# Optimization experiments

Measured on AMD Instinct MI355X. Metric: run time of the kernel, lower is better.

Reference implementation:

```python
import jax, jax.numpy as jnp
import numpy as np

REG_MAX = 16
NUM_CLASSES = 1
NUM_KPTS = 17
TOPK = 13
EPS = 1e-9

OKS_SIGMAS = np.array([0.026,0.025,0.025,0.035,0.035,0.079,0.079,0.072,0.072,0.062,0.062,0.107,0.107,0.087,0.087,0.089,0.089], np.float32)


def _bce(logits, target):
    # stable binary_cross_entropy_with_logits, reduction='none'
    return jnp.maximum(logits, 0.0) - logits * target + jnp.log1p(jnp.exp(-jnp.abs(logits)))


def _pairwise_iou(gt, pred):
    # gt [B,n,4], pred [B,L,4] -> iou [B,n,L]
    g = gt[:, :, None, :]
    p = pred[:, None, :, :]
    inter_w = jnp.clip(jnp.minimum(g[..., 2], p[..., 2]) - jnp.maximum(g[..., 0], p[..., 0]), 0.0)
    inter_h = jnp.clip(jnp.minimum(g[..., 3], p[..., 3]) - jnp.maximum(g[..., 1], p[..., 1]), 0.0)
    inter = inter_w * inter_h
    ag = (g[..., 2] - g[..., 0]) * (g[..., 3] - g[..., 1])
    ap = (p[..., 2] - p[..., 0]) * (p[..., 3] - p[..., 1])
    return inter / (ag + ap - inter + EPS)


def _assign(pred_scores_sig, pred_bboxes, anchor_points, gt_class, gt_bboxes, pad_gt_mask):
    # TaskAlignedAssigner(topk=13, alpha=1.0, beta=6.0)
    B, n, _ = gt_bboxes.shape
    L = pred_bboxes.shape[1]
    ious = _pairwise_iou(gt_bboxes, pred_bboxes)                                  # [B,n,L]
    idx = jnp.broadcast_to(gt_class, (B, n, L))
    cls = jnp.take_along_axis(jnp.swapaxes(pred_scores_sig, 1, 2), idx, axis=1)   # [B,n,L]
    metrics = cls * ious ** 6.0                                                   # alpha=1, beta=6
    ap = anchor_points[None, None, :, :]
    in_gt = ((ap[..., 0] - gt_bboxes[:, :, None, 0] > EPS)
             & (ap[..., 1] - gt_bboxes[:, :, None, 1] > EPS)
             & (gt_bboxes[:, :, None, 2] - ap[..., 0] > EPS)
             & (gt_bboxes[:, :, None, 3] - ap[..., 1] > EPS)).astype(metrics.dtype)
    _, topk_idx = jax.lax.top_k(metrics * in_gt, TOPK)                            # [B,n,K]
    topk_idx = jnp.where(pad_gt_mask > 0, topk_idx, 0)
    is_in_topk = jax.nn.one_hot(topk_idx, L, dtype=metrics.dtype).sum(-2)
    is_in_topk = jnp.where(is_in_topk > 1, 0.0, is_in_topk)
    mask_pos = is_in_topk * in_gt * pad_gt_mask                                   # [B,n,L]
    # resolve anchors assigned to multiple gts: keep gt with max iou
    is_max_iou = jnp.swapaxes(jax.nn.one_hot(ious.argmax(axis=1), n, dtype=metrics.dtype), 1, 2)
    mask_pos = jnp.where(mask_pos.sum(1, keepdims=True) > 1, is_max_iou, mask_pos)
    pos = mask_pos.sum(1) > 0                                                     # [B,L]
    assigned_gt_index = mask_pos.argmax(1)                                        # [B,L]
    bix = jnp.arange(B)[:, None]
    assigned_labels = jnp.where(pos, gt_class[bix, assigned_gt_index, 0], NUM_CLASSES)
    assigned_bboxes = gt_bboxes[bix, assigned_gt_index]                           # [B,L,4]
    one_hot_lbl = jax.nn.one_hot(assigned_labels, NUM_CLASSES + 1, dtype=metrics.dtype)[..., :NUM_CLASSES]
    # rescale alignment metrics by per-gt max iou / max metric
    m = metrics * mask_pos
    m = m / (m.max(-1, keepdims=True) + EPS) * (ious * mask_pos).max(-1, keepdims=True)
    assigned_scores = one_hot_lbl * m.max(1)[..., None]                           # [B,L,1]
    return assigned_labels, assigned_bboxes, assigned_scores, assigned_gt_index, pos


def _bbox_decode(anchor_points_s, pred_distri):
    B, L, _ = pred_distri.shape
    prob = jax.nn.softmax(pred_distri.reshape(B, L, 4, REG_MAX + 1), axis=-1)
    dist = prob @ jnp.arange(REG_MAX + 1, dtype=prob.dtype)                       # DFL projection
    return jnp.concatenate([anchor_points_s - dist[..., :2], anchor_points_s + dist[..., 2:]], -1)


def _giou(pb, gb):
    inter_w = jnp.clip(jnp.minimum(pb[..., 2], gb[..., 2]) - jnp.maximum(pb[..., 0], gb[..., 0]), 0.0)
    inter_h = jnp.clip(jnp.minimum(pb[..., 3], gb[..., 3]) - jnp.maximum(pb[..., 1], gb[..., 1]), 0.0)
    inter = inter_w * inter_h
    a1 = (pb[..., 2] - pb[..., 0]) * (pb[..., 3] - pb[..., 1])
    a2 = (gb[..., 2] - gb[..., 0]) * (gb[..., 3] - gb[..., 1])
    union = a1 + a2 - inter + EPS
    iou = inter / union
    cw = jnp.maximum(pb[..., 2], gb[..., 2]) - jnp.minimum(pb[..., 0], gb[..., 0])
    ch = jnp.maximum(pb[..., 3], gb[..., 3]) - jnp.minimum(pb[..., 1], gb[..., 1])
    area_c = cw * ch + EPS
    return 1.0 - (iou - (area_c - union) / area_c)


def _df_loss(pred_dist, target):
    # pred_dist [B,L,4,reg_max+1], target [B,L,4] in [0, reg_max-0.01]
    tl = jnp.floor(target).astype(jnp.int32)
    wl = (tl.astype(target.dtype) + 1.0) - target
    logp = jax.nn.log_softmax(pred_dist, -1)
    ll = -jnp.take_along_axis(logp, tl[..., None], -1)[..., 0]
    lr = -jnp.take_along_axis(logp, (tl + 1)[..., None], -1)[..., 0]
    return (ll * wl + lr * (1.0 - wl)).mean(-1)                                   # [B,L]


def _forward(pred_scores, pred_distri, pred_pose_logits, anchor_points, stride_tensor,
             gt_bboxes, pad_gt_mask, gt_poses, oks_sigmas, gt_class):
    B, L, _ = pred_scores.shape
    anchor_points_s = anchor_points / stride_tensor
    pred_bboxes = _bbox_decode(anchor_points_s, pred_distri)
    sgd = jax.lax.stop_gradient
    assigned_labels, assigned_bboxes, assigned_scores, assigned_gt_index, pos = _assign(
        sgd(jax.nn.sigmoid(pred_scores)), sgd(pred_bboxes * stride_tensor), anchor_points,
        gt_class, gt_bboxes, pad_gt_mask)
    assigned_bboxes = assigned_bboxes / stride_tensor
    # focal classification loss (alpha=-1 -> no alpha weighting, gamma=2)
    w = jnp.abs(jax.nn.sigmoid(pred_scores) - assigned_scores) ** 2
    ass_sum = jnp.maximum(assigned_scores.sum(), 1.0)
    loss_cls = (w * _bce(pred_scores, assigned_scores)).sum() / ass_sum
    posf = pos.astype(pred_scores.dtype)
    bbox_w = assigned_scores.sum(-1) * posf                                        # [B,L]
    loss_iou = (_giou(pred_bboxes, assigned_bboxes) * bbox_w).sum() / ass_sum
    ltrb = jnp.clip(jnp.concatenate([anchor_points_s - assigned_bboxes[..., :2],
                                     assigned_bboxes[..., 2:] - anchor_points_s], -1),
                    0.0, REG_MAX - 0.01)
    loss_dfl = (_df_loss(pred_distri.reshape(B, L, 4, REG_MAX + 1), ltrb) * bbox_w).sum() / ass_sum
    bix = jnp.arange(B)[:, None]
    kpts = gt_poses[bix, assigned_gt_index]                                        # [B,L,J,3]
    gt_xy = kpts[..., :2] / stride_tensor[None, :, None, :]
    pred_xy = pred_pose_logits[..., :2] + anchor_points_s[None, :, None, :]
    d = ((pred_xy - gt_xy) ** 2).sum(-1)                                           # [B,L,J]
    kmf = ((kpts[..., 2] != 0) & pos[..., None]).astype(d.dtype)
    area = ((assigned_bboxes[..., 2] - assigned_bboxes[..., 0])
            * (assigned_bboxes[..., 3] - assigned_bboxes[..., 1]))[..., None]
    e = d / (2.0 * oks_sigmas[None, None, :]) ** 2 / (area + EPS) / 2.0
    n_pos_kpts = jnp.maximum(posf.sum() * NUM_KPTS, 1.0)
    factor = n_pos_kpts / (kmf.sum() + EPS)
    loss_pose_reg = factor * ((1.0 - jnp.exp(-e)) * kmf).sum() / n_pos_kpts
    loss_pose_cls = (_bce(pred_pose_logits[..., 2], kmf) * posf[..., None]).sum() / n_pos_kpts
    loss = 1.0 * loss_cls + 2.5 * loss_iou + 0.5 * loss_dfl + 1.0 * loss_pose_cls + 1.0 * loss_pose_reg
    log_losses = jnp.stack([loss_cls, loss_iou, loss_dfl, loss_pose_cls, loss_pose_reg, loss])
    return loss, log_losses


def _make_anchors():
    pts, strides = [], []
    for s in (8, 16, 32):
        g = 640 // s
        xs = (np.arange(g, dtype=np.float32) + 0.5) * s
        yv, xv = np.meshgrid(xs, xs, indexing='ij')
        pts.append(np.stack([xv.ravel(), yv.ravel()], -1))
        strides.append(np.full((g * g, 1), s, np.float32))
    return jnp.asarray(np.concatenate(pts)), jnp.asarray(np.concatenate(strides))


def setup_inputs() -> dict:
    B, N, J, L = 16, 32, 17, 8400
    key = jax.random.key(0)
    ks = jax.random.split(key, 8)
    anchor_points, stride_tensor = _make_anchors()
    x1y1 = jax.random.uniform(ks[0], (B, N, 2), minval=0.0, maxval=480.0)
    wh = jax.random.uniform(ks[1], (B, N, 2), minval=32.0, maxval=160.0)
    gt_bboxes = jnp.concatenate([x1y1, x1y1 + wh], -1)
    pad_gt_mask = jnp.broadcast_to((jnp.arange(N)[None, :, None] < 24), (B, N, 1)).astype(jnp.float32)
    gt_class = jnp.zeros((B, N, 1), jnp.int32)
    ctr = x1y1 + wh / 2.0
    kxy = ctr[:, :, None, :] + jax.random.normal(ks[2], (B, N, J, 2)) * wh[:, :, None, :] * 0.2
    vis = jax.random.randint(ks[3], (B, N, J), 0, 3).astype(jnp.float32)
    gt_poses = jnp.concatenate([kxy, vis[..., None]], -1)
    pred_scores = jax.random.normal(ks[4], (B, L, 1)) * 0.5 - 2.0
    pred_distri = jax.random.normal(ks[5], (B, L, 4 * (REG_MAX + 1)))
    pred_pose_logits = jax.random.normal(ks[6], (B, L, J, 3))
    return {'pred_scores': pred_scores, 'pred_distri': pred_distri,
            'pred_pose_logits': pred_pose_logits, 'anchor_points': anchor_points,
            'stride_tensor': stride_tensor, 'gt_bboxes': gt_bboxes,
            'pad_gt_mask': pad_gt_mask, 'gt_poses': gt_poses,
            'oks_sigmas': jnp.asarray(OKS_SIGMAS), 'gt_class': gt_class}


def reference(pred_scores, pred_distri, pred_pose_logits, anchor_points, stride_tensor,
              gt_bboxes, pad_gt_mask, gt_poses, oks_sigmas, gt_class):
    return _forward(pred_scores, pred_distri, pred_pose_logits, anchor_points, stride_tensor,
                    gt_bboxes, pad_gt_mask, gt_poses, oks_sigmas, gt_class)
```

## Files before the change

### kernel.cpp

```cpp
#include <hip/hip_runtime.h>
#include <cstddef>

#define EPS 1e-9f
#define REG_MAX 16
#define TOPK 13
#define NGT 32
#define CAP 1024
#define LSLOT 16

__device__ __forceinline__ float sigmoidf(float x){ return 1.0f/(1.0f+expf(-x)); }
__device__ __forceinline__ float bcef(float l, float t){
    return fmaxf(l,0.0f) - l*t + log1pf(expf(-fabsf(l)));
}
__device__ __forceinline__ float pow6f(float x){ float x2=x*x; return x2*x2*x2; }
__device__ __forceinline__ float iou_px(float p0,float p1,float p2,float p3,
                                        float4 g, float gag){
    float iw = fmaxf(fminf(g.z,p2)-fmaxf(g.x,p0), 0.f);
    float ih = fmaxf(fminf(g.w,p3)-fmaxf(g.y,p1), 0.f);
    float inter = iw*ih;
    float ap = (p2-p0)*(p3-p1);
    return inter/(gag+ap-inter+EPS);
}

__global__ void k_zero(int* __restrict__ ccnt, unsigned int* __restrict__ rowmax_m,
                       unsigned int* __restrict__ rowmax_i, int* __restrict__ pcnt,
                       int BN)
{
    int t = threadIdx.x;
    for (int i=t; i<BN; i+=256){ ccnt[i]=0; rowmax_m[i]=0u; rowmax_i[i]=0u; }
    if (t==0) *pcnt = 0;
}

__global__ void k_main(const float* __restrict__ pred_scores,
                       const float* __restrict__ pred_distri,
                       const float* __restrict__ anchor_points,
                       const float* __restrict__ stride_t,
                       const float* __restrict__ gt_bboxes,
                       const float* __restrict__ pad_mask,
                       float* __restrict__ pred_bboxes,
                       float* __restrict__ sig_g,
                       unsigned int* __restrict__ words,
                       float2* __restrict__ cand,
                       int* __restrict__ ccnt,
                       int B,int N,int L,int nchunks)
{
    __shared__ float4 sgt[NGT];
    __shared__ float  sag[NGT];
    __shared__ int    sval[NGT];
    int b = blockIdx.x / nchunks, chunk = blockIdx.x % nchunks;
    int tid = threadIdx.x;
    if (tid < N){
        float4 g = ((const float4*)gt_bboxes)[b*N+tid];
        sgt[tid] = g;
        sag[tid] = (g.z-g.x)*(g.w-g.y);
        sval[tid] = pad_mask[b*N+tid] > 0.f ? 1 : 0;
    }
    __syncthreads();
    int l = chunk*256 + tid;
    if (l >= L) return;
    int idx = b*L + l;
    words[idx] = 0u;

    float v[68];
    const float4* pd4 = (const float4*)(pred_distri + (size_t)idx*68);
    #pragma unroll
    for (int i=0;i<17;i++){ float4 q = pd4[i]; v[4*i]=q.x; v[4*i+1]=q.y; v[4*i+2]=q.z; v[4*i+3]=q.w; }
    float dist[4];
    #pragma unroll
    for (int s=0;s<4;s++){
        float m = -1e30f;
        #pragma unroll
        for (int i=0;i<=REG_MAX;i++) m = fmaxf(m, v[s*17+i]);
        float sum=0.f, ws=0.f;
        #pragma unroll
        for (int i=0;i<=REG_MAX;i++){ float e = expf(v[s*17+i]-m); sum+=e; ws += e*(float)i; }
        dist[s] = ws/sum;
    }
    float st = stride_t[l];
    float apx = anchor_points[2*l], apy = anchor_points[2*l+1];
    float ax = apx/st, ay = apy/st;
    float4 box = make_float4(ax-dist[0], ay-dist[1], ax+dist[2], ay+dist[3]);
    ((float4*)pred_bboxes)[idx] = box;
    float sg = sigmoidf(pred_scores[idx]);
    sig_g[idx] = sg;

    float p0 = box.x*st, p1 = box.y*st, p2 = box.z*st, p3 = box.w*st;
    #pragma unroll
    for (int n=0;n<NGT;n++){
        float4 g = sgt[n];
        bool ing = (apx-g.x>EPS)&&(apy-g.y>EPS)&&(g.z-apx>EPS)&&(g.w-apy>EPS);
        if (ing && sval[n]){
            float iou = iou_px(p0,p1,p2,p3,g,sag[n]);
            float mv = sg*pow6f(iou);
            int slot = atomicAdd(&ccnt[b*N+n], 1);
            if (slot < CAP) cand[(size_t)(b*N+n)*CAP+slot] = make_float2(mv, __int_as_float(l));
        }
    }
}

__global__ void k_select(const float2* __restrict__ cand,
                         const int* __restrict__ ccnt,
                         unsigned int* __restrict__ words,
                         int B,int N,int L)
{
    int bn = blockIdx.x; int b = bn/N, n = bn%N;
    int cnt = ccnt[bn]; cnt = cnt < CAP ? cnt : CAP;
    int tid = threadIdx.x;
    unsigned int nbit = 1u<<n;
    const float2* my = cand + (size_t)bn*CAP;
    if (cnt <= TOPK){
        if (tid < cnt) atomicOr(&words[b*L + __float_as_int(my[tid].y)], nbit);
        return;
    }
    if (tid >= 64) return;
    float lv[LSLOT]; int li[LSLOT];
    #pragma unroll
    for (int k=0;k<LSLOT;k++){ lv[k]=-1.f; li[k]=0x7fffffff; }
    for (int i=tid; i<cnt; i+=64){
        float2 e = my[i];
        float cv = e.x; int ci = __float_as_int(e.y);
        #pragma unroll
        for (int k=0;k<LSLOT;k++){
            bool better = (cv>lv[k]) || (cv==lv[k] && ci<li[k]);
            if (better){
                float tv=lv[k]; lv[k]=cv; cv=tv;
                int   ti=li[k]; li[k]=ci; ci=ti;
            }
        }
    }
    for (int r=0;r<TOPK;r++){
        float bv=lv[0]; int bl=li[0];
        #pragma unroll
        for (int off=32; off>0; off>>=1){
            float ov = __shfl_xor(bv, off);
            int   oi = __shfl_xor(bl, off);
            if (ov>bv || (ov==bv && oi<bl)){ bv=ov; bl=oi; }
        }
        if (li[0]==bl){
            atomicOr(&words[b*L + bl], nbit);
            #pragma unroll
            for (int k=0;k<LSLOT-1;k++){ lv[k]=lv[k+1]; li[k]=li[k+1]; }
            lv[LSLOT-1]=-1.f; li[LSLOT-1]=0x7fffffff;
        }
    }
}

__global__ void k_resolve(const float* __restrict__ pred_bboxes,
                          const float* __restrict__ stride_t,
                          const float* __restrict__ gt_bboxes,
                          const float* __restrict__ sig,
                          unsigned int* __restrict__ words,
                          unsigned int* __restrict__ rowmax_m,
                          unsigned int* __restrict__ rowmax_i,
                          int* __restrict__ poslist,
                          int* __restrict__ pcnt,
                          int B,int N,int L)
{
    int idx = blockIdx.x*blockDim.x + threadIdx.x;
    if (idx >= B*L) return;
    int b = idx / L, l = idx % L;
    unsigned int w = words[idx];
    if (!w) return;
    float4 box = ((const float4*)pred_bboxes)[idx];
    float st = stride_t[l];
    float p0 = box.x*st, p1 = box.y*st, p2 = box.z*st, p3 = box.w*st;
    const float4* gt = (const float4*)gt_bboxes + b*N;
    int n;
    if (__popc(w) > 1){
        float bv=-1e30f; int bbest=0;
        #pragma unroll 4
        for (int nn=0;nn<NGT;nn++){
            float4 g = gt[nn];
            float vv = iou_px(p0,p1,p2,p3,g,(g.z-g.x)*(g.w-g.y));
            if (vv > bv){ bv=vv; bbest=nn; }
        }
        n = bbest;
        words[idx] = 1u<<n;
    } else {
        n = __ffs(w)-1;
    }
    float4 g = gt[n];
    float iou = iou_px(p0,p1,p2,p3,g,(g.z-g.x)*(g.w-g.y));
    float met = sig[idx]*pow6f(iou);
    atomicMax(&rowmax_m[b*N+n], __float_as_uint(met));
    atomicMax(&rowmax_i[b*N+n], __float_as_uint(iou));
    int slot = atomicAdd(pcnt, 1);
    poslist[slot] = idx;
}

__global__ void k_loss(const float* __restrict__ pred_scores,
                       const float* __restrict__ pred_distri,
                       const float* __restrict__ pose_logits,
                       const float* __restrict__ anchor_points,
                       const float* __restrict__ stride_t,
                       const float* __restrict__ gt_bboxes,
                       const float* __restrict__ gt_poses,
                       const float* __restrict__ sigmas,
                       const int*   __restrict__ gt_class,
                       const float* __restrict__ pred_bboxes,
                       const float* __restrict__ sig,
                       const unsigned int* __restrict__ words,
                       const unsigned int* __restrict__ rowmax_m,
                       const unsigned int* __restrict__ rowmax_i,
                       const int* __restrict__ poslist,
                       const int* __restrict__ pcnt,
                       float* __restrict__ partials,
                       int B,int N,int L,int J)
{
    int tid = threadIdx.x;
    float a_score=0,a_cls=0,a_giou=0,a_dfl=0,a_pos=0,a_kmf=0,a_preg=0,a_pcls=0;

    int idx = blockIdx.x*blockDim.x + tid;
    if (idx < B*L){
        int b = idx/L, l = idx%L;
        unsigned int w = words[idx];
        float assigned = 0.f;
        if (w){
            int n = __ffs(w)-1;
            float4 box = ((const float4*)pred_bboxes)[idx];
            float st = stride_t[l];
            float4 g = ((const float4*)gt_bboxes)[b*N+n];
            float iou = iou_px(box.x*st,box.y*st,box.z*st,box.w*st,
                               g,(g.z-g.x)*(g.w-g.y));
            float met = sig[idx]*pow6f(iou);
            float score = met/(__uint_as_float(rowmax_m[b*N+n])+EPS)
                          *__uint_as_float(rowmax_i[b*N+n]);
            if (gt_class[b*N+n]==0) assigned = score;
        }
        float logit = pred_scores[idx];
        float sg = sig[idx];
        float wg = sg - assigned; wg *= wg;
        a_cls = wg * bcef(logit, assigned);
        a_score = assigned;
    }

    int cnt = *pcnt;
    int e = blockIdx.x + tid*gridDim.x;
    if (e < cnt){
        int pidx = poslist[e];
        int b = pidx/L, l = pidx%L;
        int n = __ffs(words[pidx])-1;
        float st = stride_t[l];
        float4 pb = ((const float4*)pred_bboxes)[pidx];
        float4 g  = ((const float4*)gt_bboxes)[b*N+n];
        float iou0 = iou_px(pb.x*st,pb.y*st,pb.z*st,pb.w*st,
                            g,(g.z-g.x)*(g.w-g.y));
        float met = sig[pidx]*pow6f(iou0);
        float score = met/(__uint_as_float(rowmax_m[b*N+n])+EPS)
                      *__uint_as_float(rowmax_i[b*N+n]);
        float assigned = (gt_class[b*N+n]==0) ? score : 0.f;
        a_pos = 1.f;
        float ab0=g.x/st, ab1=g.y/st, ab2=g.z/st, ab3=g.w/st;
        float area = (ab2-ab0)*(ab3-ab1);
        float apx = anchor_points[2*l]/st, apy = anchor_points[2*l+1]/st;
        float bw = assigned;
        if (bw > 0.f){
            float iw = fmaxf(fminf(pb.z,ab2)-fmaxf(pb.x,ab0),0.f);
            float ih = fmaxf(fminf(pb.w,ab3)-fmaxf(pb.y,ab1),0.f);
            float inter=iw*ih;
            float a1=(pb.z-pb.x)*(pb.w-pb.y);
            float a2=(ab2-ab0)*(ab3-ab1);
            float uni=a1+a2-inter+EPS;
            float iou=inter/uni;
            float cw=fmaxf(pb.z,ab2)-fminf(pb.x,ab0);
            float ch=fmaxf(pb.w,ab3)-fminf(pb.y,ab1);
            float ac=cw*ch+EPS;
            float gg = 1.f-(iou-(ac-uni)/ac);
            a_giou = gg*bw;
            float t4[4] = { apx-ab0, apy-ab1, ab2-apx, ab3-apy };
            const float* pdist = pred_distri + (size_t)pidx*68;
            const float4* pd4 = (const float4*)pdist;
            float v[68];
            #pragma unroll
            for (int q=0;q<17;q++){ float4 qq=pd4[q]; v[4*q]=qq.x; v[4*q+1]=qq.y; v[4*q+2]=qq.z; v[4*q+3]=qq.w; }
            float dfl=0.f;
            #pragma unroll
            for (int s2=0;s2<4;s2++){
                float tt = fminf(fmaxf(t4[s2],0.f),(float)REG_MAX-0.01f);
                int tl = (int)floorf(tt);
                float wl = (float)tl + 1.f - tt;
                float m=-1e30f;
                #pragma unroll
                for (int q=0;q<=REG_MAX;q++) m=fmaxf(m,v[s2*17+q]);
                float se=0.f;
                #pragma unroll
                for (int q=0;q<=REG_MAX;q++) se+=expf(v[s2*17+q]-m);
                float lse = m + logf(se);
                float ll = -(pdist[s2*17+tl]-lse);
                float lr = -(pdist[s2*17+tl+1]-lse);
                dfl += ll*wl + lr*(1.f-wl);
            }
            a_dfl = dfl*0.25f*bw;
        }
        const float* gp = gt_poses + ((size_t)(b*N+n))*J*3;
        const float* pl = pose_logits + (size_t)pidx*J*3;
        for (int j=0;j<J;j++){
            float gx=gp[3*j]/st, gy=gp[3*j+1]/st, vis=gp[3*j+2];
            float px=pl[3*j]+apx, py=pl[3*j+1]+apy, pz=pl[3*j+2];
            float kmf = (vis!=0.f)?1.f:0.f;
            float dx=px-gx, dy=py-gy;
            float d = dx*dx+dy*dy;
            float s2g = 2.f*sigmas[j]; s2g*=s2g;
            float ee = d/s2g/(area+EPS)/2.f;
            a_preg += (1.f-expf(-ee))*kmf;
            a_kmf  += kmf;
            a_pcls += bcef(pz, kmf);
        }
    }

    float acc[8] = {a_score,a_cls,a_giou,a_dfl,a_pos,a_kmf,a_preg,a_pcls};
    #pragma unroll
    for (int k=0;k<8;k++){
        #pragma unroll
        for (int off=32; off>0; off>>=1) acc[k] += __shfl_xor(acc[k], off);
    }
    __shared__ float wsum[8][8];
    int wid = tid>>6;
    if ((tid&63)==0){
        #pragma unroll
        for (int k=0;k<8;k++) wsum[wid][k]=acc[k];
    }
    __syncthreads();
    if (tid<8){
        float s=0.f;
        #pragma unroll
        for (int i=0;i<8;i++) s += wsum[i][tid];
        partials[(size_t)blockIdx.x*8+tid]=s;
    }
}

__global__ void k_final(const float* __restrict__ partials, int nblk, int J,
                        float* __restrict__ out)
{
    __shared__ float red[256][9];
    int tid = threadIdx.x;
    float acc[8] = {0,0,0,0,0,0,0,0};
    for (int i=tid; i<nblk; i+=256){
        const float4* p = (const float4*)(partials + (size_t)i*8);
        float4 a = p[0], b = p[1];
        acc[0]+=a.x; acc[1]+=a.y; acc[2]+=a.z; acc[3]+=a.w;
        acc[4]+=b.x; acc[5]+=b.y; acc[6]+=b.z; acc[7]+=b.w;
    }
    #pragma unroll
    for (int k=0;k<8;k++) red[tid][k]=acc[k];
    __syncthreads();
    for (int s=128;s>0;s>>=1){
        if (tid<s){
            #pragma unroll
            for (int k=0;k<8;k++) red[tid][k]+=red[tid+s][k];
        }
        __syncthreads();
    }
    if (tid==0){
        float ass  = fmaxf(red[0][0],1.f);
        float lcls = red[0][1]/ass;
        float liou = red[0][2]/ass;
        float ldfl = red[0][3]/ass;
        float npk  = fmaxf(red[0][4]*(float)J,1.f);
        float factor = npk/(red[0][5]+EPS);
        float preg = factor*red[0][6]/npk;
        float pcls = red[0][7]/npk;
        float loss = lcls + 2.5f*liou + 0.5f*ldfl + pcls + preg;
        out[0]=loss; out[1]=lcls; out[2]=liou; out[3]=ldfl;
        out[4]=pcls; out[5]=preg; out[6]=loss;
    }
}

extern "C" void kernel_launch(void* const* d_in, const int* in_sizes, int n_in,
                              void* d_out, int out_size, void* d_ws, size_t ws_size,
                              hipStream_t stream)
{
    const float* pred_scores   = (const float*)d_in[0];
    const float* pred_distri   = (const float*)d_in[1];
    const float* pose_logits   = (const float*)d_in[2];
    const float* anchor_points = (const float*)d_in[3];
    const float* stride_t      = (const float*)d_in[4];
    const float* gt_bboxes     = (const float*)d_in[5];
    const float* pad_mask      = (const float*)d_in[6];
    const float* gt_poses      = (const float*)d_in[7];
    const float* sigmas        = (const float*)d_in[8];
    const int*   gt_class      = (const int*)d_in[9];

    int L = in_sizes[3]/2;
    int B = in_sizes[0]/L;
    int N = in_sizes[5]/(B*4);
    int J = in_sizes[8];

    char* ws = (char*)d_ws;
    size_t off=0;
    auto alloc=[&](size_t bytes)->void*{
        size_t cur=off; off += (bytes+255)/256*256; return (void*)(ws+cur);
    };
    float* pred_bboxes    = (float*)alloc((size_t)B*L*4*4);
    float* sig            = (float*)alloc((size_t)B*L*4);
    unsigned int* words   = (unsigned int*)alloc((size_t)B*L*4);
    unsigned int* rowmax_m= (unsigned int*)alloc((size_t)B*N*4);
    unsigned int* rowmax_i= (unsigned int*)alloc((size_t)B*N*4);
    float2* cand          = (float2*)alloc((size_t)B*N*CAP*8);
    int* ccnt             = (int*)alloc((size_t)B*N*4);
    int maxpos = B*N*TOPK;
    int* poslist          = (int*)alloc((size_t)maxpos*4);
    int* pcnt             = (int*)alloc(256);
    int nchunks  = (L+255)/256;
    int nblkR    = (B*L+255)/256;
    int nblkL    = (B*L+511)/512;
    float* partials       = (float*)alloc((size_t)nblkL*8*4);
    (void)ws_size; (void)n_in; (void)out_size;

    k_zero<<<1,256,0,stream>>>(ccnt,rowmax_m,rowmax_i,pcnt,B*N);
    k_main<<<B*nchunks,256,0,stream>>>(pred_scores,pred_distri,anchor_points,
                                       stride_t,gt_bboxes,pad_mask,
                                       pred_bboxes,sig,words,cand,ccnt,
                                       B,N,L,nchunks);
    k_select<<<B*N,256,0,stream>>>(cand,ccnt,words,B,N,L);
    k_resolve<<<nblkR,256,0,stream>>>(pred_bboxes,stride_t,gt_bboxes,sig,
                                      words,rowmax_m,rowmax_i,
                                      poslist,pcnt,B,N,L);
    k_loss<<<nblkL,512,0,stream>>>(pred_scores,pred_distri,pose_logits,
                                   anchor_points,stride_t,gt_bboxes,gt_poses,
                                   sigmas,gt_class,pred_bboxes,sig,
                                   words,rowmax_m,rowmax_i,poslist,pcnt,
                                   partials,B,N,L,J);
    k_final<<<1,256,0,stream>>>(partials,nblkL,J,(float*)d_out);
}
```

Baseline: 97.77 us.

## Replace global candidate atomics with per-block segmented lists and fuse final reduction

Candidate collection in the main kernel now uses wave ballots and per-block shared counters, writing into per-chunk segments instead of global atomics on one list per gt. The select kernel prefix-sums the chunk counts and also does the zeroing that a separate kernel used to do. The final reduction is folded into the loss kernel with a last-block ticket, and the loss block size changes to 256. These remove two launches and global atomic contention, at the cost of a serial prefix scan per gt and a linear segment search per element. The segment capacity of 256 is tied to the 256-thread chunk size.

```diff
diff --git a/kernel.cpp b/kernel.cpp
--- a/kernel.cpp
+++ b/kernel.cpp
@@ -5,7 +5,7 @@
 #define REG_MAX 16
 #define TOPK 13
 #define NGT 32
-#define CAP 1024
+#define SEGCAP 256
 #define LSLOT 16
 
 __device__ __forceinline__ float sigmoidf(float x){ return 1.0f/(1.0f+expf(-x)); }
@@ -20,15 +20,6 @@
     float inter = iw*ih;
     float ap = (p2-p0)*(p3-p1);
     return inter/(gag+ap-inter+EPS);
-}
-
-__global__ void k_zero(int* __restrict__ ccnt, unsigned int* __restrict__ rowmax_m,
-                       unsigned int* __restrict__ rowmax_i, int* __restrict__ pcnt,
-                       int BN)
-{
-    int t = threadIdx.x;
-    for (int i=t; i<BN; i+=256){ ccnt[i]=0; rowmax_m[i]=0u; rowmax_i[i]=0u; }
-    if (t==0) *pcnt = 0;
 }
 
 __global__ void k_main(const float* __restrict__ pred_scores,
@@ -40,84 +31,119 @@
                        float* __restrict__ pred_bboxes,
                        float* __restrict__ sig_g,
                        unsigned int* __restrict__ words,
-                       float2* __restrict__ cand,
-                       int* __restrict__ ccnt,
+                       float2* __restrict__ cand2,
+                       int* __restrict__ cnts2,
                        int B,int N,int L,int nchunks)
 {
     __shared__ float4 sgt[NGT];
     __shared__ float  sag[NGT];
     __shared__ int    sval[NGT];
-    int b = blockIdx.x / nchunks, chunk = blockIdx.x % nchunks;
+    __shared__ int    lcnt[NGT];
+    int bc = blockIdx.x;
+    int b = bc / nchunks, chunk = bc % nchunks;
     int tid = threadIdx.x;
     if (tid < N){
         float4 g = ((const float4*)gt_bboxes)[b*N+tid];
         sgt[tid] = g;
         sag[tid] = (g.z-g.x)*(g.w-g.y);
         sval[tid] = pad_mask[b*N+tid] > 0.f ? 1 : 0;
+        lcnt[tid] = 0;
     }
     __syncthreads();
     int l = chunk*256 + tid;
-    if (l >= L) return;
-    int idx = b*L + l;
-    words[idx] = 0u;
-
-    float v[68];
-    const float4* pd4 = (const float4*)(pred_distri + (size_t)idx*68);
-    #pragma unroll
-    for (int i=0;i<17;i++){ float4 q = pd4[i]; v[4*i]=q.x; v[4*i+1]=q.y; v[4*i+2]=q.z; v[4*i+3]=q.w; }
-    float dist[4];
-    #pragma unroll
-    for (int s=0;s<4;s++){
-        float m = -1e30f;
-        #pragma unroll
-        for (int i=0;i<=REG_MAX;i++) m = fmaxf(m, v[s*17+i]);
-        float sum=0.f, ws=0.f;
-        #pragma unroll
-        for (int i=0;i<=REG_MAX;i++){ float e = expf(v[s*17+i]-m); sum+=e; ws += e*(float)i; }
-        dist[s] = ws/sum;
-    }
-    float st = stride_t[l];
-    float apx = anchor_points[2*l], apy = anchor_points[2*l+1];
-    float ax = apx/st, ay = apy/st;
-    float4 box = make_float4(ax-dist[0], ay-dist[1], ax+dist[2], ay+dist[3]);
-    ((float4*)pred_bboxes)[idx] = box;
-    float sg = sigmoidf(pred_scores[idx]);
-    sig_g[idx] = sg;
-
-    float p0 = box.x*st, p1 = box.y*st, p2 = box.z*st, p3 = box.w*st;
-    #pragma unroll
+    bool active = (l < L);
+    float sg=0.f, p0=0,p1=0,p2=0,p3=0, apx=0, apy=0;
+    if (active){
+        int idx = b*L + l;
+        words[idx] = 0u;
+        float v[68];
+        const float4* pd4 = (const float4*)(pred_distri + (size_t)idx*68);
+        #pragma unroll
+        for (int i=0;i<17;i++){ float4 q = pd4[i]; v[4*i]=q.x; v[4*i+1]=q.y; v[4*i+2]=q.z; v[4*i+3]=q.w; }
+        float dist[4];
+        #pragma unroll
+        for (int s=0;s<4;s++){
+            float m = -1e30f;
+            #pragma unroll
+            for (int i=0;i<=REG_MAX;i++) m = fmaxf(m, v[s*17+i]);
+            float sum=0.f, ws=0.f;
+            #pragma unroll
+            for (int i=0;i<=REG_MAX;i++){ float e = expf(v[s*17+i]-m); sum+=e; ws += e*(float)i; }
+            dist[s] = ws/sum;
+        }
+        float st = stride_t[l];
+        apx = anchor_points[2*l]; apy = anchor_points[2*l+1];
+        float ax = apx/st, ay = apy/st;
+        float4 box = make_float4(ax-dist[0], ay-dist[1], ax+dist[2], ay+dist[3]);
+        ((float4*)pred_bboxes)[idx] = box;
+        sg = sigmoidf(pred_scores[idx]);
+        sig_g[idx] = sg;
+        p0 = box.x*st; p1 = box.y*st; p2 = box.z*st; p3 = box.w*st;
+    }
+    unsigned long long lmask_lt = ((tid&63)==0) ? 0ull
+                                : ((~0ull) >> (64-(tid&63)));
+    #pragma unroll 4
     for (int n=0;n<NGT;n++){
         float4 g = sgt[n];
-        bool ing = (apx-g.x>EPS)&&(apy-g.y>EPS)&&(g.z-apx>EPS)&&(g.w-apy>EPS);
-        if (ing && sval[n]){
-            float iou = iou_px(p0,p1,p2,p3,g,sag[n]);
-            float mv = sg*pow6f(iou);
-            int slot = atomicAdd(&ccnt[b*N+n], 1);
-            if (slot < CAP) cand[(size_t)(b*N+n)*CAP+slot] = make_float2(mv, __int_as_float(l));
-        }
-    }
-}
-
-__global__ void k_select(const float2* __restrict__ cand,
-                         const int* __restrict__ ccnt,
+        bool want = active && sval[n] &&
+                    (apx-g.x>EPS)&&(apy-g.y>EPS)&&(g.z-apx>EPS)&&(g.w-apy>EPS);
+        unsigned long long mask = __ballot(want);
+        if (mask){
+            int leader = __ffsll(mask)-1;
+            int base = 0;
+            if ((tid&63)==leader) base = atomicAdd(&lcnt[n], __popcll(mask));
+            base = __shfl(base, leader);
+            if (want){
+                int rank = __popcll(mask & lmask_lt);
+                float iou = iou_px(p0,p1,p2,p3,g,sag[n]);
+                float mv = sg*pow6f(iou);
+                cand2[((size_t)bc*NGT + n)*SEGCAP + base + rank] =
+                    make_float2(mv, __int_as_float(l));
+            }
+        }
+    }
+    __syncthreads();
+    if (tid < N) cnts2[bc*NGT + tid] = lcnt[tid];
+}
+
+__global__ void k_select(const float2* __restrict__ cand2,
+                         const int* __restrict__ cnts2,
                          unsigned int* __restrict__ words,
-                         int B,int N,int L)
+                         unsigned int* __restrict__ rowmax_m,
+                         unsigned int* __restrict__ rowmax_i,
+                         int* __restrict__ pcnt,
+                         int B,int N,int L,int nchunks)
 {
+    __shared__ int soff[64];
     int bn = blockIdx.x; int b = bn/N, n = bn%N;
-    int cnt = ccnt[bn]; cnt = cnt < CAP ? cnt : CAP;
     int tid = threadIdx.x;
+    if (tid==0){
+        rowmax_m[bn]=0u; rowmax_i[bn]=0u;
+        if (bn==0) *pcnt = 0;
+        int acc=0;
+        for (int c=0;c<nchunks;c++){
+            soff[c]=acc; acc += cnts2[(b*nchunks+c)*NGT + n];
+        }
+        soff[nchunks]=acc;
+    }
+    __syncthreads();
+    int total = soff[nchunks];
     unsigned int nbit = 1u<<n;
-    const float2* my = cand + (size_t)bn*CAP;
-    if (cnt <= TOPK){
-        if (tid < cnt) atomicOr(&words[b*L + __float_as_int(my[tid].y)], nbit);
+    if (total <= TOPK){
+        if (tid < total){
+            int c=0; while (soff[c+1] <= tid) c++;
+            float2 e = cand2[((size_t)(b*nchunks+c)*NGT + n)*SEGCAP + tid - soff[c]];
+            atomicOr(&words[b*L + __float_as_int(e.y)], nbit);
+        }
         return;
     }
     if (tid >= 64) return;
     float lv[LSLOT]; int li[LSLOT];
     #pragma unroll
     for (int k=0;k<LSLOT;k++){ lv[k]=-1.f; li[k]=0x7fffffff; }
-    for (int i=tid; i<cnt; i+=64){
-        float2 e = my[i];
+    for (int i=tid; i<total; i+=64){
+        int c=0; while (soff[c+1] <= i) c++;
+        float2 e = cand2[((size_t)(b*nchunks+c)*NGT + n)*SEGCAP + i - soff[c]];
         float cv = e.x; int ci = __float_as_int(e.y);
         #pragma unroll
         for (int k=0;k<LSLOT;k++){
@@ -154,9 +180,11 @@
                           unsigned int* __restrict__ rowmax_i,
                           int* __restrict__ poslist,
                           int* __restrict__ pcnt,
+                          unsigned int* __restrict__ ticket,
                           int B,int N,int L)
 {
     int idx = blockIdx.x*blockDim.x + threadIdx.x;
+    if (idx == 0) *ticket = 0u;
     if (idx >= B*L) return;
     int b = idx / L, l = idx % L;
     unsigned int w = words[idx];
@@ -205,6 +233,8 @@
                        const int* __restrict__ poslist,
                        const int* __restrict__ pcnt,
                        float* __restrict__ partials,
+                       unsigned int* __restrict__ ticket,
+                       float* __restrict__ out,
                        int B,int N,int L,int J)
 {
     int tid = threadIdx.x;
@@ -234,77 +264,78 @@
         a_score = assigned;
     }
 
-    int cnt = *pcnt;
-    int e = blockIdx.x + tid*gridDim.x;
-    if (e < cnt){
-        int pidx = poslist[e];
-        int b = pidx/L, l = pidx%L;
-        int n = __ffs(words[pidx])-1;
-        float st = stride_t[l];
-        float4 pb = ((const float4*)pred_bboxes)[pidx];
-        float4 g  = ((const float4*)gt_bboxes)[b*N+n];
-        float iou0 = iou_px(pb.x*st,pb.y*st,pb.z*st,pb.w*st,
-                            g,(g.z-g.x)*(g.w-g.y));
-        float met = sig[pidx]*pow6f(iou0);
-        float score = met/(__uint_as_float(rowmax_m[b*N+n])+EPS)
-                      *__uint_as_float(rowmax_i[b*N+n]);
-        float assigned = (gt_class[b*N+n]==0) ? score : 0.f;
-        a_pos = 1.f;
-        float ab0=g.x/st, ab1=g.y/st, ab2=g.z/st, ab3=g.w/st;
-        float area = (ab2-ab0)*(ab3-ab1);
-        float apx = anchor_points[2*l]/st, apy = anchor_points[2*l+1]/st;
-        float bw = assigned;
-        if (bw > 0.f){
-            float iw = fmaxf(fminf(pb.z,ab2)-fmaxf(pb.x,ab0),0.f);
-            float ih = fmaxf(fminf(pb.w,ab3)-fmaxf(pb.y,ab1),0.f);
-            float inter=iw*ih;
-            float a1=(pb.z-pb.x)*(pb.w-pb.y);
-            float a2=(ab2-ab0)*(ab3-ab1);
-            float uni=a1+a2-inter+EPS;
-            float iou=inter/uni;
-            float cw=fmaxf(pb.z,ab2)-fminf(pb.x,ab0);
-            float ch=fmaxf(pb.w,ab3)-fminf(pb.y,ab1);
-            float ac=cw*ch+EPS;
-            float gg = 1.f-(iou-(ac-uni)/ac);
-            a_giou = gg*bw;
-            float t4[4] = { apx-ab0, apy-ab1, ab2-apx, ab3-apy };
-            const float* pdist = pred_distri + (size_t)pidx*68;
-            const float4* pd4 = (const float4*)pdist;
-            float v[68];
-            #pragma unroll
-            for (int q=0;q<17;q++){ float4 qq=pd4[q]; v[4*q]=qq.x; v[4*q+1]=qq.y; v[4*q+2]=qq.z; v[4*q+3]=qq.w; }
-            float dfl=0.f;
-            #pragma unroll
-            for (int s2=0;s2<4;s2++){
-                float tt = fminf(fmaxf(t4[s2],0.f),(float)REG_MAX-0.01f);
-                int tl = (int)floorf(tt);
-                float wl = (float)tl + 1.f - tt;
-                float m=-1e30f;
+    {
+        int cnt = *pcnt;
+        for (int e = blockIdx.x + tid*gridDim.x; e < cnt; e += gridDim.x*blockDim.x){
+            int pidx = poslist[e];
+            int b = pidx/L, l = pidx%L;
+            int n = __ffs(words[pidx])-1;
+            float st = stride_t[l];
+            float4 pb = ((const float4*)pred_bboxes)[pidx];
+            float4 g  = ((const float4*)gt_bboxes)[b*N+n];
+            float iou0 = iou_px(pb.x*st,pb.y*st,pb.z*st,pb.w*st,
+                                g,(g.z-g.x)*(g.w-g.y));
+            float met = sig[pidx]*pow6f(iou0);
+            float score = met/(__uint_as_float(rowmax_m[b*N+n])+EPS)
+                          *__uint_as_float(rowmax_i[b*N+n]);
+            float assigned = (gt_class[b*N+n]==0) ? score : 0.f;
+            a_pos += 1.f;
+            float ab0=g.x/st, ab1=g.y/st, ab2=g.z/st, ab3=g.w/st;
+            float area = (ab2-ab0)*(ab3-ab1);
+            float apx = anchor_points[2*l]/st, apy = anchor_points[2*l+1]/st;
+            float bw = assigned;
+            if (bw > 0.f){
+                float iw = fmaxf(fminf(pb.z,ab2)-fmaxf(pb.x,ab0),0.f);
+                float ih = fmaxf(fminf(pb.w,ab3)-fmaxf(pb.y,ab1),0.f);
+                float inter=iw*ih;
+                float a1=(pb.z-pb.x)*(pb.w-pb.y);
+                float a2=(ab2-ab0)*(ab3-ab1);
+                float uni=a1+a2-inter+EPS;
+                float iou=inter/uni;
+                float cw=fmaxf(pb.z,ab2)-fminf(pb.x,ab0);
+                float ch=fmaxf(pb.w,ab3)-fminf(pb.y,ab1);
+                float ac=cw*ch+EPS;
+                float gg = 1.f-(iou-(ac-uni)/ac);
+                a_giou += gg*bw;
+                float t4[4] = { apx-ab0, apy-ab1, ab2-apx, ab3-apy };
+                const float* pdist = pred_distri + (size_t)pidx*68;
+                const float4* pd4 = (const float4*)pdist;
+                float v[68];
                 #pragma unroll
-                for (int q=0;q<=REG_MAX;q++) m=fmaxf(m,v[s2*17+q]);
-                float se=0.f;
+                for (int q=0;q<17;q++){ float4 qq=pd4[q]; v[4*q]=qq.x; v[4*q+1]=qq.y; v[4*q+2]=qq.z; v[4*q+3]=qq.w; }
+                float dfl=0.f;
                 #pragma unroll
-                for (int q=0;q<=REG_MAX;q++) se+=expf(v[s2*17+q]-m);
-                float lse = m + logf(se);
-                float ll = -(pdist[s2*17+tl]-lse);
-                float lr = -(pdist[s2*17+tl+1]-lse);
-                dfl += ll*wl + lr*(1.f-wl);
+                for (int s2=0;s2<4;s2++){
+                    float tt = fminf(fmaxf(t4[s2],0.f),(float)REG_MAX-0.01f);
+                    int tl = (int)floorf(tt);
+                    float wl = (float)tl + 1.f - tt;
+                    float m=-1e30f;
+                    #pragma unroll
+                    for (int q=0;q<=REG_MAX;q++) m=fmaxf(m,v[s2*17+q]);
+                    float se=0.f;
+                    #pragma unroll
+                    for (int q=0;q<=REG_MAX;q++) se+=expf(v[s2*17+q]-m);
+                    float lse = m + logf(se);
+                    float ll = -(pdist[s2*17+tl]-lse);
+                    float lr = -(pdist[s2*17+tl+1]-lse);
+                    dfl += ll*wl + lr*(1.f-wl);
+                }
+                a_dfl += dfl*0.25f*bw;
             }
-            a_dfl = dfl*0.25f*bw;
-        }
-        const float* gp = gt_poses + ((size_t)(b*N+n))*J*3;
-        const float* pl = pose_logits + (size_t)pidx*J*3;
-        for (int j=0;j<J;j++){
-            float gx=gp[3*j]/st, gy=gp[3*j+1]/st, vis=gp[3*j+2];
-            float px=pl[3*j]+apx, py=pl[3*j+1]+apy, pz=pl[3*j+2];
-            float kmf = (vis!=0.f)?1.f:0.f;
-            float dx=px-gx, dy=py-gy;
-            float d = dx*dx+dy*dy;
-            float s2g = 2.f*sigmas[j]; s2g*=s2g;
-            float ee = d/s2g/(area+EPS)/2.f;
-            a_preg += (1.f-expf(-ee))*kmf;
-            a_kmf  += kmf;
-            a_pcls += bcef(pz, kmf);
+            const float* gp = gt_poses + ((size_t)(b*N+n))*J*3;
+            const float* pl = pose_logits + (size_t)pidx*J*3;
+            for (int j=0;j<J;j++){
+                float gx=gp[3*j]/st, gy=gp[3*j+1]/st, vis=gp[3*j+2];
+                float px=pl[3*j]+apx, py=pl[3*j+1]+apy, pz=pl[3*j+2];
+                float kmf = (vis!=0.f)?1.f:0.f;
+                float dx=px-gx, dy=py-gy;
+                float d = dx*dx+dy*dy;
+                float s2g = 2.f*sigmas[j]; s2g*=s2g;
+                float ee = d/s2g/(area+EPS)/2.f;
+                a_preg += (1.f-expf(-ee))*kmf;
+                a_kmf  += kmf;
+                a_pcls += bcef(pz, kmf);
+            }
         }
     }
 
@@ -315,6 +346,7 @@
         for (int off=32; off>0; off>>=1) acc[k] += __shfl_xor(acc[k], off);
     }
     __shared__ float wsum[8][8];
+    __shared__ int s_last;
     int wid = tid>>6;
     if ((tid&63)==0){
         #pragma unroll
@@ -323,48 +355,61 @@
     __syncthreads();
     if (tid<8){
         float s=0.f;
-        #pragma unroll
-        for (int i=0;i<8;i++) s += wsum[i][tid];
+        int nw = blockDim.x>>6;
+        for (int i=0;i<nw;i++) s += wsum[i][tid];
         partials[(size_t)blockIdx.x*8+tid]=s;
     }
-}
-
-__global__ void k_final(const float* __restrict__ partials, int nblk, int J,
-                        float* __restrict__ out)
-{
-    __shared__ float red[256][9];
-    int tid = threadIdx.x;
-    float acc[8] = {0,0,0,0,0,0,0,0};
-    for (int i=tid; i<nblk; i+=256){
-        const float4* p = (const float4*)(partials + (size_t)i*8);
-        float4 a = p[0], b = p[1];
-        acc[0]+=a.x; acc[1]+=a.y; acc[2]+=a.z; acc[3]+=a.w;
-        acc[4]+=b.x; acc[5]+=b.y; acc[6]+=b.z; acc[7]+=b.w;
-    }
-    #pragma unroll
-    for (int k=0;k<8;k++) red[tid][k]=acc[k];
+    __threadfence();
+    if (tid==0){
+        unsigned int t = atomicAdd(ticket, 1u);
+        s_last = (t == gridDim.x-1u) ? 1 : 0;
+    }
     __syncthreads();
-    for (int s=128;s>0;s>>=1){
-        if (tid<s){
+    if (!s_last) return;
+    {
+        float fin[8] = {0,0,0,0,0,0,0,0};
+        __shared__ float red[256][9];
+        for (int i=tid; i<(int)gridDim.x; i+=blockDim.x){
+            const float4* p = (const float4*)(partials + (size_t)i*8);
+            float4 a = p[0], bq = p[1];
+            fin[0]+=a.x; fin[1]+=a.y; fin[2]+=a.z; fin[3]+=a.w;
+            fin[4]+=bq.x; fin[5]+=bq.y; fin[6]+=bq.z; fin[7]+=bq.w;
+        }
+        if (tid<256){
             #pragma unroll
-            for (int k=0;k<8;k++) red[tid][k]+=red[tid+s][k];
+            for (int k=0;k<8;k++) red[tid][k]= (tid<blockDim.x)?fin[k]:0.f;
         }
         __syncthreads();
-    }
-    if (tid==0){
-        float ass  = fmaxf(red[0][0],1.f);
-        float lcls = red[0][1]/ass;
-        float liou = red[0][2]/ass;
-        float ldfl = red[0][3]/ass;
-        float npk  = fmaxf(red[0][4]*(float)J,1.f);
-        float factor = npk/(red[0][5]+EPS);
-        float preg = factor*red[0][6]/npk;
-        float pcls = red[0][7]/npk;
-        float loss = lcls + 2.5f*liou + 0.5f*ldfl + pcls + preg;
-        out[0]=loss; out[1]=lcls; out[2]=liou; out[3]=ldfl;
-        out[4]=pcls; out[5]=preg; out[6]=loss;
-    }
-}
+        if (tid>=256){
+            #pragma unroll
+            for (int k=0;k<8;k++) atomicAdd(&red[tid-256][k], 0.f);
+        }
+        __syncthreads();
+        if (tid<256 && blockDim.x>256){
+        }
+        for (int s=128;s>0;s>>=1){
+            if (tid<s){
+                #pragma unroll
+                for (int k=0;k<8;k++) red[tid][k]+=red[tid+s][k];
+            }
+            __syncthreads();
+        }
+        if (tid==0){
+            float ass  = fmaxf(red[0][0],1.f);
+            float lcls = red[0][1]/ass;
+            float liou = red[0][2]/ass;
+            float ldfl = red[0][3]/ass;
+            float npk  = fmaxf(red[0][4]*(float)J,1.f);
+            float factor = npk/(red[0][5]+EPS);
+            float preg = factor*red[0][6]/npk;
+            float pcls = red[0][7]/npk;
+            float loss = lcls + 2.5f*liou + 0.5f*ldfl + pcls + preg;
+            out[0]=loss; out[1]=lcls; out[2]=liou; out[3]=ldfl;
+            out[4]=pcls; out[5]=preg; out[6]=loss;
+        }
+    }
+}
+
 
 extern "C" void kernel_launch(void* const* d_in, const int* in_sizes, int n_in,
                               void* d_out, int out_size, void* d_ws, size_t ws_size,
@@ -391,35 +436,34 @@
     auto alloc=[&](size_t bytes)->void*{
         size_t cur=off; off += (bytes+255)/256*256; return (void*)(ws+cur);
     };
+    int nchunks = (L+255)/256;
     float* pred_bboxes    = (float*)alloc((size_t)B*L*4*4);
     float* sig            = (float*)alloc((size_t)B*L*4);
     unsigned int* words   = (unsigned int*)alloc((size_t)B*L*4);
     unsigned int* rowmax_m= (unsigned int*)alloc((size_t)B*N*4);
     unsigned int* rowmax_i= (unsigned int*)alloc((size_t)B*N*4);
-    float2* cand          = (float2*)alloc((size_t)B*N*CAP*8);
-    int* ccnt             = (int*)alloc((size_t)B*N*4);
+    float2* cand2         = (float2*)alloc((size_t)B*nchunks*NGT*SEGCAP*8);
+    int* cnts2            = (int*)alloc((size_t)B*nchunks*NGT*4);
     int maxpos = B*N*TOPK;
     int* poslist          = (int*)alloc((size_t)maxpos*4);
     int* pcnt             = (int*)alloc(256);
-    int nchunks  = (L+255)/256;
-    int nblkR    = (B*L+255)/256;
-    int nblkL    = (B*L+511)/512;
+    unsigned int* ticket  = (unsigned int*)alloc(256);
+    int nblkL = (B*L+255)/256;
     float* partials       = (float*)alloc((size_t)nblkL*8*4);
     (void)ws_size; (void)n_in; (void)out_size;
 
-    k_zero<<<1,256,0,stream>>>(ccnt,rowmax_m,rowmax_i,pcnt,B*N);
     k_main<<<B*nchunks,256,0,stream>>>(pred_scores,pred_distri,anchor_points,
                                        stride_t,gt_bboxes,pad_mask,
-                                       pred_bboxes,sig,words,cand,ccnt,
+                                       pred_bboxes,sig,words,cand2,cnts2,
                                        B,N,L,nchunks);
-    k_select<<<B*N,256,0,stream>>>(cand,ccnt,words,B,N,L);
-    k_resolve<<<nblkR,256,0,stream>>>(pred_bboxes,stride_t,gt_bboxes,sig,
-                                      words,rowmax_m,rowmax_i,
-                                      poslist,pcnt,B,N,L);
-    k_loss<<<nblkL,512,0,stream>>>(pred_scores,pred_distri,pose_logits,
+    k_select<<<B*N,256,0,stream>>>(cand2,cnts2,words,rowmax_m,rowmax_i,pcnt,
+                                   B,N,L,nchunks);
+    k_resolve<<<(B*L+255)/256,256,0,stream>>>(pred_bboxes,stride_t,gt_bboxes,
+                                              sig,words,rowmax_m,rowmax_i,
+                                              poslist,pcnt,ticket,B,N,L);
+    k_loss<<<nblkL,256,0,stream>>>(pred_scores,pred_distri,pose_logits,
                                    anchor_points,stride_t,gt_bboxes,gt_poses,
                                    sigmas,gt_class,pred_bboxes,sig,
                                    words,rowmax_m,rowmax_i,poslist,pcnt,
-                                   partials,B,N,L,J);
-    k_final<<<1,256,0,stream>>>(partials,nblkL,J,(float*)d_out);
-}
+                                   partials,ticket,(float*)d_out,B,N,L,J);
+}
```

Result: slower. 137.7 us (+40.8%).
